# Optimization experiments

Measured on AMD Instinct MI355X. Metric: run time of the kernel, lower is better.

The kernel has to match this reference:

```python
import jax, jax.numpy as jnp
import numpy as np

EPS = 1e-5

def gru_step(x, h, Wih, Whh, bih, bhh):
    # PyTorch GRU cell math. x:[B,C], h:[B,H], Wih:[3H,C], Whh:[3H,H]
    gi = x @ Wih.T + bih
    gh = h @ Whh.T + bhh
    ir, iz, inn = jnp.split(gi, 3, axis=-1)
    hr, hz, hn = jnp.split(gh, 3, axis=-1)
    r = jax.nn.sigmoid(ir + hr)
    z = jax.nn.sigmoid(iz + hz)
    n = jnp.tanh(inn + r * hn)
    return (1.0 - z) * n + z * h

def batchnorm_train(x, g, b):
    # x:[B,C]; training-mode BN over batch dim, biased variance
    mu = jnp.mean(x, axis=0)
    var = jnp.mean((x - mu) ** 2, axis=0)
    return g * (x - mu) / jnp.sqrt(var + EPS) + b

def setup_inputs() -> dict:
    B, Le, T = 256, 1024, 48
    Fe, Fd, G, R, H = 16, 16, 32, 16, 256
    Ce, Cd = Fe + R, Fd + R + 1  # 32, 33
    key = jax.random.key(0)
    ks = jax.random.split(key, 24)
    s = 0.05
    inp = {
        "X_Encoder": jax.random.normal(ks[0], (B, Le, Fe), jnp.float32),
        "X_Decoder": jax.random.normal(ks[1], (B, T, Fd), jnp.float32),
        "Xg_Encoder": jax.random.normal(ks[2], (B, Le, G), jnp.float32),
        "Xg_Decoder": jax.random.normal(ks[3], (B, T, G), jnp.float32),
        # global feature reducers
        "Wg_enc": jax.random.normal(ks[4], (R, G), jnp.float32) * s,
        "bg_enc": jnp.zeros((R,), jnp.float32),
        "Wg_dec": jax.random.normal(ks[5], (R, G), jnp.float32) * s,
        "bg_dec": jnp.zeros((R,), jnp.float32),
        # encoder GRU + output head
        "enc_Wih": jax.random.normal(ks[6], (3 * H, Ce), jnp.float32) * s,
        "enc_Whh": jax.random.normal(ks[7], (3 * H, H), jnp.float32) * s,
        "enc_bih": jnp.zeros((3 * H,), jnp.float32),
        "enc_bhh": jnp.zeros((3 * H,), jnp.float32),
        "enc_Wo": jax.random.normal(ks[8], (1, H), jnp.float32) * s,
        "enc_bo": jnp.zeros((1,), jnp.float32),
        # decoder GRU + output head
        "dec_Wih": jax.random.normal(ks[9], (3 * H, Cd), jnp.float32) * s,
        "dec_Whh": jax.random.normal(ks[10], (3 * H, H), jnp.float32) * s,
        "dec_bih": jnp.zeros((3 * H,), jnp.float32),
        "dec_bhh": jnp.zeros((3 * H,), jnp.float32),
        "dec_Wo": jax.random.normal(ks[11], (1, H), jnp.float32) * s,
        "dec_bo": jnp.zeros((1,), jnp.float32),
        # BatchNorm params: BN_1 and per-step BN_layers (T of them)
        "bn1_g": jnp.ones((Cd,), jnp.float32),
        "bn1_b": jnp.zeros((Cd,), jnp.float32),
        "bnT_g": jnp.ones((T, Cd), jnp.float32),
        "bnT_b": jnp.zeros((T, Cd), jnp.float32),
    }
    return inp

def reference(X_Encoder, X_Decoder, Xg_Encoder, Xg_Decoder,
              Wg_enc, bg_enc, Wg_dec, bg_dec,
              enc_Wih, enc_Whh, enc_bih, enc_bhh, enc_Wo, enc_bo,
              dec_Wih, dec_Whh, dec_bih, dec_bhh, dec_Wo, dec_bo,
              bn1_g, bn1_b, bnT_g, bnT_b):
    B, Le, _ = X_Encoder.shape
    T = X_Decoder.shape[1]
    H = enc_Whh.shape[1]
    # batched global-feature reduction (replaces nested per-element loops)
    enc_in = jnp.concatenate([X_Encoder, Xg_Encoder @ Wg_enc.T + bg_enc], axis=2)  # [B,Le,Ce]
    dec_wg = jnp.concatenate([X_Decoder, Xg_Decoder @ Wg_dec.T + bg_dec], axis=2)  # [B,T,Fd+R]
    # encoder: sequential GRU over Le steps
    def estep(h, x):
        return gru_step(x, h, enc_Wih, enc_Whh, enc_bih, enc_bhh), None
    h0 = jnp.zeros((B, H), enc_in.dtype)
    h_enc, _ = jax.lax.scan(estep, h0, jnp.swapaxes(enc_in, 0, 1))
    enc_out = h_enc @ enc_Wo.T + enc_bo  # [B,1]
    # first decoder input: concat + BN_1 (train mode); dropout p=0 -> identity
    dec_in0 = batchnorm_train(jnp.concatenate([dec_wg[:, 0], enc_out], axis=1), bn1_g, bn1_b)
    # next-step exogenous inputs, padded with zeros for the (unused) last step
    next_x = jnp.concatenate([dec_wg[:, 1:], jnp.zeros((B, 1, dec_wg.shape[2]), dec_wg.dtype)], axis=1)
    next_x = jnp.swapaxes(next_x, 0, 1)  # [T,B,Fd+R]
    def dstep(carry, xs):
        h, dinp = carry
        nx, g, b = xs
        h = gru_step(dinp, h, dec_Wih, dec_Whh, dec_bih, dec_bhh)
        out = h @ dec_Wo.T + dec_bo  # [B,1]
        new_in = batchnorm_train(jnp.concatenate([nx, out], axis=1), g, b)
        return (h, new_in), out
    (_, _), outs = jax.lax.scan(dstep, (h_enc, dec_in0), (next_x, bnT_g, bnT_b))
    return jnp.swapaxes(outs, 0, 1)  # [B,T,1]
```

## Files before the change

kernel.cpp:

```cpp
#include <hip/hip_runtime.h>
#include <math.h>

typedef _Float16 f16;
typedef _Float16 f16x8 __attribute__((ext_vector_type(8)));
typedef float f32x4 __attribute__((ext_vector_type(4)));

#define MFMA16(A_, B_, C_) __builtin_amdgcn_mfma_f32_16x16x32_f16((A_), (B_), (C_), 0, 0, 0)
#define SWZ(m) ((((m) & 7) ^ (((m) & 8) >> 2)) << 4)

__device__ __forceinline__ float rcpf_(float x) { return __builtin_amdgcn_rcpf(x); }
__device__ __forceinline__ float rsqf_(float x) { return __builtin_amdgcn_rsqf(x); }
__device__ __forceinline__ float sigf(float x) { return rcpf_(1.0f + __expf(-x)); }
__device__ __forceinline__ float tanhf_(float x) { return 1.0f - 2.0f * rcpf_(__expf(2.0f * x) + 1.0f); }

static const size_t OFF_ENCIN = 0;
static const size_t OFF_DECIN = 16777216;
static const size_t OFF_WENC  = OFF_DECIN + 786432;
static const size_t OFF_WDEC  = OFF_WENC + 442368;
static const size_t OFF_W32   = OFF_WDEC + 442368;
static const size_t OFF_BE    = OFF_W32 + 3072;
static const size_t OFF_BD    = OFF_BE + 4096;
static const size_t OFF_HENC  = OFF_BD + 4096;
static const size_t OFF_EOUT  = OFF_HENC + 131072;
static const size_t OFF_XST   = OFF_EOUT + 1024;
static const size_t OFF_OST   = OFF_XST + 12288;
static const size_t OFF_CNT   = OFF_OST + 512;

struct P {
  const float *Xe, *Xd, *Xge, *Xgd, *Wge, *bge, *Wgd, *bgd;
  const float *eWih, *eWhh, *ebih, *ebhh, *eWo, *ebo;
  const float *dWih, *dWhh, *dbih, *dbhh, *dWo, *dbo;
  const float *bn1g, *bn1b, *bnTg, *bnTb;
  f16 *encin, *decin, *wencf, *wdecf;
  float *w32, *bE, *bD;
  f16 *henc;
  float *eout, *xst, *ost;
  int *cnt;
  float *out;
};

__global__ void prep1(P p) {
  const int blk = blockIdx.x, tid = threadIdx.x;
  __shared__ float swg[512];
  __shared__ float sbg[16];
  if (blk < 1024) {
    for (int i = tid; i < 512; i += 256) swg[i] = p.Wge[i];
    if (tid < 16) sbg[tid] = p.bge[tid];
    __syncthreads();
    const int i = blk * 256 + tid;
    const int b = i >> 10, t = i & 1023;
    const float* xg = p.Xge + (size_t)(b * 1024 + t) * 32;
    const float* xe = p.Xe + (size_t)(b * 1024 + t) * 16;
    f16* o = p.encin + (size_t)(t * 256 + b) * 32;
    float xgv[32];
#pragma unroll
    for (int k = 0; k < 32; ++k) xgv[k] = xg[k];
#pragma unroll
    for (int c = 0; c < 16; ++c) o[c] = (f16)xe[c];
#pragma unroll 4
    for (int r = 0; r < 16; ++r) {
      float acc = sbg[r];
#pragma unroll
      for (int k = 0; k < 32; ++k) acc += swg[r * 32 + k] * xgv[k];
      o[16 + r] = (f16)acc;
    }
  } else if (blk < 1072) {
    for (int i = tid; i < 512; i += 256) swg[i] = p.Wgd[i];
    if (tid < 16) sbg[tid] = p.bgd[tid];
    __syncthreads();
    const int i = (blk - 1024) * 256 + tid;
// ... 29 lines not shown
    const int kt = i / 3072, r2 = i - kt * 3072;
    const int nt = r2 >> 6, l = r2 & 63;
    const int n = nt * 16 + (l & 15), g = l >> 4;
    f16* o = p.wdecf + (size_t)i * 8;
#pragma unroll
    for (int j = 0; j < 8; ++j) {
      const int k = g * 8 + j;
      o[j] = (f16)((kt == 0) ? p.dWih[n * 33 + k] : p.dWhh[n * 256 + (kt - 1) * 32 + k]);
    }
  } else if (blk == 1288) {
    for (int i = tid; i < 768; i += 256) p.w32[i] = p.dWih[i * 33 + 32];
    for (int i = tid; i < 128; i += 256) p.ost[i] = 0.f;
    if (tid < 64) p.cnt[tid] = 0;
  } else if (blk == 1289) {
    for (int i = tid; i < 1024; i += 256) {
      float v;
      if (i < 512) v = p.ebih[i] + p.ebhh[i];
      else if (i < 768) v = p.ebih[i];
      else v = p.ebhh[i - 256];
      p.bE[i] = v;
    }
  } else {
    for (int i = tid; i < 1024; i += 256) {
      float v;
      if (i < 512) v = p.dbih[i] + p.dbhh[i];
      else if (i < 768) v = p.dbih[i];
      else v = p.dbhh[i - 256];
      p.bD[i] = v;
    }
  }
}

__global__ void prep2(P p) {
  const int i = blockIdx.x * 256 + threadIdx.x;
  if (i >= 48 * 32) return;
  const int s = i >> 5, c = i & 31;
  float s1 = 0.f, s2 = 0.f;
  for (int b = 0; b < 256; ++b) {
    const float v = (float)p.decin[(size_t)(s * 256 + b) * 32 + c];
    s1 += v; s2 += v * v;
  }
  const float mu = s1 * (1.0f / 256.0f);
  p.xst[i * 2] = mu;
  p.xst[i * 2 + 1] = s2 * (1.0f / 256.0f) - mu * mu;
}

__global__ __launch_bounds__(512, 2) void enc_kernel(P p) {
  __shared__ f16 sWL[49152];
  __shared__ f16 sH[8192];
  __shared__ float sRed[512];
  const int tid = threadIdx.x;
  const int l = tid & 63, w = tid >> 6;
  const int g = l >> 4, m16 = l & 15;
  const int swzA = SWZ(m16);
  const int bg = blockIdx.x * 16;

  {
    const int4* src = (const int4*)(p.wencf + 172032);
    int4* dst = (int4*)sWL;
#pragma unroll
    for (int i = 0; i < 12; ++i) dst[tid + i * 512] = src[tid + i * 512];
  }
  {
    int* hz = (int*)sH;
#pragma unroll
    for (int i = 0; i < 8; ++i) hz[tid + i * 512] = 0;
  }
  const int nts[6] = {w, 8 + w, 16 + w, 24 + w, 32 + w, 40 + w};
  f16x8 Wr[7][6];
#pragma unroll
  for (int kt = 0; kt < 7; ++kt)
#pragma unroll
    for (int i = 0; i < 6; ++i)
      Wr[kt][i] = *(const f16x8*)(p.wencf + ((size_t)(kt * 48 + nts[i]) * 64 + l) * 8);
  const int J1 = 16 * w + m16, J2 = 128 + J1;
  const float br1 = p.bE[J1], bz1 = p.bE[256 + J1], bi1 = p.bE[512 + J1], bh1 = p.bE[768 + J1];
  const float br2 = p.bE[J2], bz2 = p.bE[256 + J2], bi2 = p.bE[512 + J2], bh2 = p.bE[768 + J2];
  float hp1[4] = {0.f, 0.f, 0.f, 0.f}, hp2[4] = {0.f, 0.f, 0.f, 0.f};
  __syncthreads();

  int ph = 0;
  f16x8 xf = *(const f16x8*)(p.encin + (size_t)(bg + m16) * 32 + 8 * g);
#pragma unroll 1
  for (int t = 0; t < 1024; ++t) {
    const int tn = (t < 1023) ? t + 1 : t;
    const f16x8 xn = *(const f16x8*)(p.encin + (size_t)(tn * 256 + bg + m16) * 32 + 8 * g);
    f32x4 aR0 = {br1, br1, br1, br1}, aR1 = {br2, br2, br2, br2};
    f32x4 aZ0 = {bz1, bz1, bz1, bz1}, aZ1 = {bz2, bz2, bz2, bz2};
    f32x4 aNi0 = {bi1, bi1, bi1, bi1}, aNi1 = {bi2, bi2, bi2, bi2};
    f32x4 aNh0 = {bh1, bh1, bh1, bh1}, aNh1 = {bh2, bh2, bh2, bh2};
    aR0 = MFMA16(xf, Wr[0][0], aR0);
    aR1 = MFMA16(xf, Wr[0][1], aR1);
    aZ0 = MFMA16(xf, Wr[0][2], aZ0);
    aZ1 = MFMA16(xf, Wr[0][3], aZ1);
    aNi0 = MFMA16(xf, Wr[0][4], aNi0);
    aNi1 = MFMA16(xf, Wr[0][5], aNi1);
#pragma unroll
    for (int kk = 1; kk <= 6; ++kk) {
      const f16x8 a = *(const f16x8*)((const char*)sH + ph * 8192 + m16 * 512 +
                                      ((64 * (kk - 1) + 16 * g) ^ swzA));
      aR0 = MFMA16(a, Wr[kk][0], aR0);
      aR1 = MFMA16(a, Wr[kk][1], aR1);
      aZ0 = MFMA16(a, Wr[kk][2], aZ0);
      aZ1 = MFMA16(a, Wr[kk][3], aZ1);
      aNh0 = MFMA16(a, Wr[kk][4], aNh0);
      aNh1 = MFMA16(a, Wr[kk][5], aNh1);
    }
#pragma unroll
    for (int kk = 7; kk <= 8; ++kk) {
      const f16x8 a = *(const f16x8*)((const char*)sH + ph * 8192 + m16 * 512 +
                                      ((64 * (kk - 1) + 16 * g) ^ swzA));
      const char* wb = (const char*)sWL + (kk - 7) * 49152;
      const f16x8 q0 = *(const f16x8*)(wb + (nts[0] * 64 + l) * 16);
      const f16x8 q1 = *(const f16x8*)(wb + (nts[1] * 64 + l) * 16);
      const f16x8 q2 = *(const f16x8*)(wb + (nts[2] * 64 + l) * 16);
      const f16x8 q3 = *(const f16x8*)(wb + (nts[3] * 64 + l) * 16);
      const f16x8 q4 = *(const f16x8*)(wb + (nts[4] * 64 + l) * 16);
      const f16x8 q5 = *(const f16x8*)(wb + (nts[5] * 64 + l) * 16);
      aR0 = MFMA16(a, q0, aR0);
      aR1 = MFMA16(a, q1, aR1);
      aZ0 = MFMA16(a, q2, aZ0);
      aZ1 = MFMA16(a, q3, aZ1);
      aNh0 = MFMA16(a, q4, aNh0);
      aNh1 = MFMA16(a, q5, aNh1);
    }
    {
      char* hw = (char*)sH + (ph ^ 1) * 8192;
#pragma unroll
      for (int q = 0; q < 4; ++q) {
        const int m = 4 * g + q;
        const int sw = SWZ(m);
        const float r1 = sigf(aR0[q]);
        const float z1 = sigf(aZ0[q]);
        const float n1 = tanhf_(aNi0[q] + r1 * aNh0[q]);
        const f16 h1 = (f16)(n1 + z1 * (hp1[q] - n1));
        hp1[q] = (float)h1;
        *(f16*)(hw + m * 512 + ((2 * J1) ^ sw)) = h1;
        const float r2 = sigf(aR1[q]);
        const float z2 = sigf(aZ1[q]);
        const float n2 = tanhf_(aNi1[q] + r2 * aNh1[q]);
        const f16 h2 = (f16)(n2 + z2 * (hp2[q] - n2));
        hp2[q] = (float)h2;
        *(f16*)(hw + m * 512 + ((2 * J2) ^ sw)) = h2;
      }
    }
    __syncthreads();
    ph ^= 1;
    xf = xn;
  }
  {
    const char* hb = (const char*)sH + ph * 8192;
    const int m = tid & 15, grp = tid >> 4;
    const f16x8 hv = *(const f16x8*)(hb + m * 512 + ((16 * grp) ^ SWZ(m)));
    *(f16x8*)(p.henc + (size_t)(bg + m) * 256 + 8 * grp) = hv;
    float part = 0.f;
#pragma unroll
    for (int jj = 0; jj < 8; ++jj) part += (float)hv[jj] * p.eWo[8 * grp + jj];
    sRed[m * 32 + grp] = part;
    __syncthreads();
    if (tid < 16) {
      float o = p.ebo[0];
#pragma unroll 8
      for (int k = 0; k < 32; ++k) o += sRed[tid * 32 + k];
      p.eout[bg + tid] = o;
    }
  }
}

__global__ __launch_bounds__(512, 2) void dec_kernel(P p) {
  __shared__ f16 sWL[49152];
  __shared__ f16 sH[8192];
  __shared__ f16 sDin[1024];
  __shared__ float sRed[512];
  __shared__ float sOutv[16];
  __shared__ float sO32[16];
  const int tid = threadIdx.x;
  const int l = tid & 63, w = tid >> 6;
  const int g = l >> 4, m16 = l & 15;
  const int sw16 = (m16 & 7) << 4;
  const int swzA = SWZ(m16);
  const int bg = blockIdx.x * 16;

  {
    const int4* src = (const int4*)(p.wdecf + 172032);
    int4* dst = (int4*)sWL;
#pragma unroll
    for (int i = 0; i < 12; ++i) dst[tid + i * 512] = src[tid + i * 512];
  }
  {
    const int m = tid & 15, grp = tid >> 4;
    const f16x8 hv = *(const f16x8*)(p.henc + (size_t)(bg + m) * 256 + 8 * grp);
    *(f16x8*)((char*)sH + m * 512 + ((16 * grp) ^ SWZ(m))) = hv;
  }
  if (tid < 128) ((int4*)sDin)[tid] = int4{0, 0, 0, 0};
  const int nts[6] = {w, 8 + w, 16 + w, 24 + w, 32 + w, 40 + w};
  f16x8 Wr[7][6];
#pragma unroll
  for (int kt = 0; kt < 7; ++kt)
#pragma unroll
    for (int i = 0; i < 6; ++i)
      Wr[kt][i] = *(const f16x8*)(p.wdecf + ((size_t)(kt * 48 + nts[i]) * 64 + l) * 8);
  const int J1 = 16 * w + m16, J2 = 128 + J1;
  const float br1 = p.bD[J1], bz1 = p.bD[256 + J1], bi1 = p.bD[512 + J1], bh1 = p.bD[768 + J1];
  const float br2 = p.bD[J2], bz2 = p.bD[256 + J2], bi2 = p.bD[512 + J2], bh2 = p.bD[768 + J2];
  const float w32r1 = p.w32[J1], w32z1 = p.w32[256 + J1], w32n1 = p.w32[512 + J1];
  const float w32r2 = p.w32[J2], w32z2 = p.w32[256 + J2], w32n2 = p.w32[512 + J2];
  float hp1[4], hp2[4];
#pragma unroll
  for (int q = 0; q < 4; ++q) {
    hp1[q] = (float)p.henc[(size_t)(bg + 4 * g + q) * 256 + J1];
    hp2[q] = (float)p.henc[(size_t)(bg + 4 * g + q) * 256 + J2];
  }
  if (tid < 16) sOutv[tid] = p.eout[bg + tid];
  __syncthreads();
  if (tid == 0) {
    float s1 = 0.f, s2 = 0.f;
#pragma unroll
    for (int k = 0; k < 16; ++k) { const float v = sOutv[k]; s1 += v; s2 += v * v; }
    atomicAdd(&p.ost[0], s1);
    atomicAdd(&p.ost[1], s2);
    __hip_atomic_fetch_add(&p.cnt[0], 1, __ATOMIC_RELEASE, __HIP_MEMORY_SCOPE_AGENT);
  }

  int ph = 0;
#pragma unroll 1
  for (int t = 0; t < 48; ++t) {
    const int mp = tid & 15, cp = tid >> 4;
    const float xq = (float)p.decin[((size_t)t * 256 + bg + mp) * 32 + cp];
    const float mx = p.xst[(t * 32 + cp) * 2], vx = p.xst[(t * 32 + cp) * 2 + 1];
    const float gc = (t == 0) ? p.bn1g[cp] : p.bnTg[(t - 1) * 33 + cp];
    const float bc = (t == 0) ? p.bn1b[cp] : p.bnTb[(t - 1) * 33 + cp];
    float gK = 0.f, bK = 0.f;
    if (tid < 16) {
      gK = (t == 0) ? p.bn1g[32] : p.bnTg[(t - 1) * 33 + 32];
      bK = (t == 0) ? p.bn1b[32] : p.bnTb[(t - 1) * 33 + 32];
    }
    f32x4 aR0 = {br1, br1, br1, br1}, aR1 = {br2, br2, br2, br2};
    f32x4 aZ0 = {bz1, bz1, bz1, bz1}, aZ1 = {bz2, bz2, bz2, bz2};
    f32x4 aNi0 = {bi1, bi1, bi1, bi1}, aNi1 = {bi2, bi2, bi2, bi2};
    f32x4 aNh0 = {bh1, bh1, bh1, bh1}, aNh1 = {bh2, bh2, bh2, bh2};
#pragma unroll
    for (int kk = 1; kk <= 6; ++kk) {
      const f16x8 a = *(const f16x8*)((const char*)sH + ph * 8192 + m16 * 512 +
                                      ((64 * (kk - 1) + 16 * g) ^ swzA));
      aR0 = MFMA16(a, Wr[kk][0], aR0);
      aR1 = MFMA16(a, Wr[kk][1], aR1);
      aZ0 = MFMA16(a, Wr[kk][2], aZ0);
      aZ1 = MFMA16(a, Wr[kk][3], aZ1);
      aNh0 = MFMA16(a, Wr[kk][4], aNh0);
      aNh1 = MFMA16(a, Wr[kk][5], aNh1);
    }
#pragma unroll
    for (int kk = 7; kk <= 8; ++kk) {
      const f16x8 a = *(const f16x8*)((const char*)sH + ph * 8192 + m16 * 512 +
                                      ((64 * (kk - 1) + 16 * g) ^ swzA));
      const char* wb = (const char*)sWL + (kk - 7) * 49152;
      const f16x8 q0 = *(const f16x8*)(wb + (nts[0] * 64 + l) * 16);
      const f16x8 q1 = *(const f16x8*)(wb + (nts[1] * 64 + l) * 16);
      const f16x8 q2 = *(const f16x8*)(wb + (nts[2] * 64 + l) * 16);
      const f16x8 q3 = *(const f16x8*)(wb + (nts[3] * 64 + l) * 16);
      const f16x8 q4 = *(const f16x8*)(wb + (nts[4] * 64 + l) * 16);
      const f16x8 q5 = *(const f16x8*)(wb + (nts[5] * 64 + l) * 16);
      aR0 = MFMA16(a, q0, aR0);
      aR1 = MFMA16(a, q1, aR1);
      aZ0 = MFMA16(a, q2, aZ0);
      aZ1 = MFMA16(a, q3, aZ1);
      aNh0 = MFMA16(a, q4, aNh0);
      aNh1 = MFMA16(a, q5, aNh1);
    }
    if (tid == 0) {
      while (__hip_atomic_load(&p.cnt[t], __ATOMIC_ACQUIRE, __HIP_MEMORY_SCOPE_AGENT) < 16)
        __builtin_amdgcn_s_sleep(1);
    }
    __syncthreads();
    if (tid < 16) {
      const float S1 = __hip_atomic_load(&p.ost[2 * t], __ATOMIC_RELAXED, __HIP_MEMORY_SCOPE_AGENT);
      const float S2 = __hip_atomic_load(&p.ost[2 * t + 1], __ATOMIC_RELAXED, __HIP_MEMORY_SCOPE_AGENT);
      const float mu = S1 * (1.0f / 256.0f);
      const float var = S2 * (1.0f / 256.0f) - mu * mu;
      sO32[tid] = gK * (sOutv[tid] - mu) * rsqf_(var + 1e-5f) + bK;
    }
    *(f16*)((char*)sDin + mp * 128 + ((2 * cp) ^ ((mp & 7) << 4))) =
        (f16)(gc * (xq - mx) * rsqf_(vx + 1e-5f) + bc);
    __syncthreads();
    {
      const f16x8 a = *(const f16x8*)((const char*)sDin + m16 * 128 + ((16 * g) ^ sw16));
      aR0 = MFMA16(a, Wr[0][0], aR0);
      aR1 = MFMA16(a, Wr[0][1], aR1);
      aZ0 = MFMA16(a, Wr[0][2], aZ0);
      aZ1 = MFMA16(a, Wr[0][3], aZ1);
      aNi0 = MFMA16(a, Wr[0][4], aNi0);
      aNi1 = MFMA16(a, Wr[0][5], aNi1);
    }
    {
      char* hw = (char*)sH + (ph ^ 1) * 8192;
#pragma unroll
      for (int q = 0; q < 4; ++q) {
        const int m = 4 * g + q;
        const int sw = SWZ(m);
        const float o32m = sO32[m];
        const float r1 = sigf(aR0[q] + o32m * w32r1);
        const float z1 = sigf(aZ0[q] + o32m * w32z1);
        const float n1 = tanhf_(aNi0[q] + o32m * w32n1 + r1 * aNh0[q]);
        const f16 h1 = (f16)(n1 + z1 * (hp1[q] - n1));
        hp1[q] = (float)h1;
        *(f16*)(hw + m * 512 + ((2 * J1) ^ sw)) = h1;
        const float r2 = sigf(aR1[q] + o32m * w32r2);
        const float z2 = sigf(aZ1[q] + o32m * w32z2);
        const float n2 = tanhf_(aNi1[q] + o32m * w32n2 + r2 * aNh1[q]);
        const f16 h2 = (f16)(n2 + z2 * (hp2[q] - n2));
        hp2[q] = (float)h2;
        *(f16*)(hw + m * 512 + ((2 * J2) ^ sw)) = h2;
      }
    }
    __syncthreads();
    {
      const int m = tid & 15, grp = tid >> 4;
      const char* hb = (const char*)sH + (ph ^ 1) * 8192;
      const f16x8 hv = *(const f16x8*)(hb + m * 512 + ((16 * grp) ^ SWZ(m)));
      float part = 0.f;
#pragma unroll
      for (int jj = 0; jj < 8; ++jj) part += (float)hv[jj] * p.dWo[8 * grp + jj];
      sRed[m * 32 + grp] = part;
    }
    __syncthreads();
    if (tid < 16) {
      float o = p.dbo[0];
#pragma unroll 8
      for (int k = 0; k < 32; ++k) o += sRed[tid * 32 + k];
      p.out[(size_t)(bg + tid) * 48 + t] = o;
      sOutv[tid] = o;
    }
    __syncthreads();
    if (t < 47 && tid == 0) {
      float s1 = 0.f, s2 = 0.f;
#pragma unroll
      for (int k = 0; k < 16; ++k) { const float v = sOutv[k]; s1 += v; s2 += v * v; }
      atomicAdd(&p.ost[2 * (t + 1)], s1);
      atomicAdd(&p.ost[2 * (t + 1) + 1], s2);
      __hip_atomic_fetch_add(&p.cnt[t + 1], 1, __ATOMIC_RELEASE, __HIP_MEMORY_SCOPE_AGENT);
    }
    ph ^= 1;
  }
}

extern "C" void kernel_launch(void* const* d_in, const int* in_sizes, int n_in,
                              void* d_out, int out_size, void* d_ws, size_t ws_size,
                              hipStream_t stream) {
  char* ws = (char*)d_ws;
// ... 4 lines not shown
  p.Xgd  = (const float*)d_in[3];
  p.Wge  = (const float*)d_in[4];
  p.bge  = (const float*)d_in[5];
  p.Wgd  = (const float*)d_in[6];
  p.bgd  = (const float*)d_in[7];
  p.eWih = (const float*)d_in[8];
  p.eWhh = (const float*)d_in[9];
  p.ebih = (const float*)d_in[10];
  p.ebhh = (const float*)d_in[11];
  p.eWo  = (const float*)d_in[12];
  p.ebo  = (const float*)d_in[13];
  p.dWih = (const float*)d_in[14];
  p.dWhh = (const float*)d_in[15];
  p.dbih = (const float*)d_in[16];
  p.dbhh = (const float*)d_in[17];
  p.dWo  = (const float*)d_in[18];
  p.dbo  = (const float*)d_in[19];
  p.bn1g = (const float*)d_in[20];
  p.bn1b = (const float*)d_in[21];
  p.bnTg = (const float*)d_in[22];
  p.bnTb = (const float*)d_in[23];
  p.encin = (f16*)(ws + OFF_ENCIN);
  p.decin = (f16*)(ws + OFF_DECIN);
  p.wencf = (f16*)(ws + OFF_WENC);
  p.wdecf = (f16*)(ws + OFF_WDEC);
  p.w32   = (float*)(ws + OFF_W32);
  p.bE    = (float*)(ws + OFF_BE);
  p.bD    = (float*)(ws + OFF_BD);
  p.henc  = (f16*)(ws + OFF_HENC);
  p.eout  = (float*)(ws + OFF_EOUT);
  p.xst   = (float*)(ws + OFF_XST);
  p.ost   = (float*)(ws + OFF_OST);
  p.cnt   = (int*)(ws + OFF_CNT);
  p.out   = (float*)d_out;

  prep1<<<dim3(1291), dim3(256), 0, stream>>>(p);
  prep2<<<dim3(6), dim3(256), 0, stream>>>(p);
  enc_kernel<<<dim3(16), dim3(512), 0, stream>>>(p);
  dec_kernel<<<dim3(16), dim3(512), 0, stream>>>(p);
}
```

Measured before the change: 3.677 ms.

## Stream spilled GRU weight tiles from global memory instead of LDS

Drops the LDS copy of the last two K-tiles of the recurrent weights in the encoder and decoder. prep2 now writes those tiles into a per-wave contiguous global layout, duplicated twice so that ph*49152 offsets index a valid copy. The loop loads them into registers at the top of each step, which frees LDS and lets the load latency overlap the earlier MFMAs. Biases move out of the accumulator initialisation into the gate math, and the input MFMA moves after the recurrent MFMAs. The cost is a global or L2 load per step on the serial critical path and higher register pressure.

Result: faster. 3.381 ms (-8.0%).

```diff
diff --git a/kernel.cpp b/kernel.cpp
--- a/kernel.cpp
+++ b/kernel.cpp
@@ -25,6 +25,8 @@
 static const size_t OFF_XST   = OFF_EOUT + 1024;
 static const size_t OFF_OST   = OFF_XST + 12288;
 static const size_t OFF_CNT   = OFF_OST + 512;
+static const size_t OFF_WSE   = OFF_CNT + 256;
+static const size_t OFF_WSD   = OFF_WSE + 196608;
 
 struct P {
   const float *Xe, *Xd, *Xge, *Xgd, *Wge, *bge, *Wgd, *bgd;
@@ -36,6 +38,7 @@
   f16 *henc;
   float *eout, *xst, *ost;
   int *cnt;
+  f16 *wse, *wsd;
   float *out;
 };
 
@@ -131,21 +134,38 @@
 }
 
 __global__ void prep2(P p) {
-  const int i = blockIdx.x * 256 + threadIdx.x;
-  if (i >= 48 * 32) return;
-  const int s = i >> 5, c = i & 31;
-  float s1 = 0.f, s2 = 0.f;
-  for (int b = 0; b < 256; ++b) {
-    const float v = (float)p.decin[(size_t)(s * 256 + b) * 32 + c];
-    s1 += v; s2 += v * v;
-  }
-  const float mu = s1 * (1.0f / 256.0f);
-  p.xst[i * 2] = mu;
-  p.xst[i * 2 + 1] = s2 * (1.0f / 256.0f) - mu * mu;
+  const int blk = blockIdx.x, tid = threadIdx.x;
+  if (blk < 6) {
+    const int i = blk * 256 + tid;
+    if (i >= 48 * 32) return;
+    const int s = i >> 5, c = i & 31;
+    float s1 = 0.f, s2 = 0.f;
+    for (int b = 0; b < 256; ++b) {
+      const float v = (float)p.decin[(size_t)(s * 256 + b) * 32 + c];
+      s1 += v; s2 += v * v;
+    }
+    const float mu = s1 * (1.0f / 256.0f);
+    p.xst[i * 2] = mu;
+    p.xst[i * 2 + 1] = s2 * (1.0f / 256.0f) - mu * mu;
+  } else {
+    const int idx = (blk - 6) * 256 + tid;
+    const int sel = idx >= 6144;
+    const int fi = sel ? idx - 6144 : idx;
+    const int wv = fi / 768;
+    const int r = fi - wv * 768;
+    const int i8 = r >> 6, l = r & 63;
+    const int kt = (i8 >= 6) ? 8 : 7;
+    const int j = (i8 >= 6) ? i8 - 6 : i8;
+    const int nt = j * 8 + wv;
+    const f16* src = (sel ? p.wdecf : p.wencf) + ((size_t)((kt * 48 + nt) * 64 + l)) * 8;
+    f16* dst = (sel ? p.wsd : p.wse) + (size_t)fi * 8;
+    const f16x8 v = *(const f16x8*)src;
+    *(f16x8*)dst = v;
+    *(f16x8*)(dst + 49152) = v;
+  }
 }
 
 __global__ __launch_bounds__(512, 2) void enc_kernel(P p) {
-  __shared__ f16 sWL[49152];
   __shared__ f16 sH[8192];
   __shared__ float sRed[512];
   const int tid = threadIdx.x;
@@ -155,12 +175,6 @@
   const int bg = blockIdx.x * 16;
 
   {
-    const int4* src = (const int4*)(p.wencf + 172032);
-    int4* dst = (int4*)sWL;
-#pragma unroll
-    for (int i = 0; i < 12; ++i) dst[tid + i * 512] = src[tid + i * 512];
-  }
-  {
     int* hz = (int*)sH;
 #pragma unroll
     for (int i = 0; i < 8; ++i) hz[tid + i * 512] = 0;
@@ -172,6 +186,9 @@
 #pragma unroll
     for (int i = 0; i < 6; ++i)
       Wr[kt][i] = *(const f16x8*)(p.wencf + ((size_t)(kt * 48 + nts[i]) * 64 + l) * 8);
+  const f16* sb0 = p.wse + ((size_t)(w * 12 + 0) * 64 + l) * 8;
+  const f16* sb1 = p.wse + ((size_t)(w * 12 + 4) * 64 + l) * 8;
+  const f16* sb2 = p.wse + ((size_t)(w * 12 + 8) * 64 + l) * 8;
   const int J1 = 16 * w + m16, J2 = 128 + J1;
   const float br1 = p.bE[J1], bz1 = p.bE[256 + J1], bi1 = p.bE[512 + J1], bh1 = p.bE[768 + J1];
   const float br2 = p.bE[J2], bz2 = p.bE[256 + J2], bi2 = p.bE[512 + J2], bh2 = p.bE[768 + J2];
@@ -179,21 +196,19 @@
   __syncthreads();
 
   int ph = 0;
-  f16x8 xf = *(const f16x8*)(p.encin + (size_t)(bg + m16) * 32 + 8 * g);
 #pragma unroll 1
   for (int t = 0; t < 1024; ++t) {
-    const int tn = (t < 1023) ? t + 1 : t;
-    const f16x8 xn = *(const f16x8*)(p.encin + (size_t)(tn * 256 + bg + m16) * 32 + 8 * g);
-    f32x4 aR0 = {br1, br1, br1, br1}, aR1 = {br2, br2, br2, br2};
-    f32x4 aZ0 = {bz1, bz1, bz1, bz1}, aZ1 = {bz2, bz2, bz2, bz2};
-    f32x4 aNi0 = {bi1, bi1, bi1, bi1}, aNi1 = {bi2, bi2, bi2, bi2};
-    f32x4 aNh0 = {bh1, bh1, bh1, bh1}, aNh1 = {bh2, bh2, bh2, bh2};
-    aR0 = MFMA16(xf, Wr[0][0], aR0);
-    aR1 = MFMA16(xf, Wr[0][1], aR1);
-    aZ0 = MFMA16(xf, Wr[0][2], aZ0);
-    aZ1 = MFMA16(xf, Wr[0][3], aZ1);
-    aNi0 = MFMA16(xf, Wr[0][4], aNi0);
-    aNi1 = MFMA16(xf, Wr[0][5], aNi1);
+    const int so = ph * 49152;
+    f16x8 qW[12];
+#pragma unroll
+    for (int k = 0; k < 4; ++k) qW[k] = *(const f16x8*)(sb0 + so + k * 512);
+#pragma unroll
+    for (int k = 0; k < 4; ++k) qW[4 + k] = *(const f16x8*)(sb1 + so + k * 512);
+#pragma unroll
+    for (int k = 0; k < 4; ++k) qW[8 + k] = *(const f16x8*)(sb2 + so + k * 512);
+    const f16x8 xf = *(const f16x8*)(p.encin + ((size_t)t * 256 + bg + m16) * 32 + 8 * g);
+    f32x4 aR0 = {0,0,0,0}, aR1 = {0,0,0,0}, aZ0 = {0,0,0,0}, aZ1 = {0,0,0,0};
+    f32x4 aNh0 = {0,0,0,0}, aNh1 = {0,0,0,0};
 #pragma unroll
     for (int kk = 1; kk <= 6; ++kk) {
       const f16x8 a = *(const f16x8*)((const char*)sH + ph * 8192 + m16 * 512 +
@@ -209,35 +224,36 @@
     for (int kk = 7; kk <= 8; ++kk) {
       const f16x8 a = *(const f16x8*)((const char*)sH + ph * 8192 + m16 * 512 +
                                       ((64 * (kk - 1) + 16 * g) ^ swzA));
-      const char* wb = (const char*)sWL + (kk - 7) * 49152;
-      const f16x8 q0 = *(const f16x8*)(wb + (nts[0] * 64 + l) * 16);
-      const f16x8 q1 = *(const f16x8*)(wb + (nts[1] * 64 + l) * 16);
-      const f16x8 q2 = *(const f16x8*)(wb + (nts[2] * 64 + l) * 16);
-      const f16x8 q3 = *(const f16x8*)(wb + (nts[3] * 64 + l) * 16);
-      const f16x8 q4 = *(const f16x8*)(wb + (nts[4] * 64 + l) * 16);
-      const f16x8 q5 = *(const f16x8*)(wb + (nts[5] * 64 + l) * 16);
-      aR0 = MFMA16(a, q0, aR0);
-      aR1 = MFMA16(a, q1, aR1);
-      aZ0 = MFMA16(a, q2, aZ0);
-      aZ1 = MFMA16(a, q3, aZ1);
-      aNh0 = MFMA16(a, q4, aNh0);
-      aNh1 = MFMA16(a, q5, aNh1);
-    }
+      const int qb = (kk - 7) * 6;
+      aR0 = MFMA16(a, qW[qb + 0], aR0);
+      aR1 = MFMA16(a, qW[qb + 1], aR1);
+      aZ0 = MFMA16(a, qW[qb + 2], aZ0);
+      aZ1 = MFMA16(a, qW[qb + 3], aZ1);
+      aNh0 = MFMA16(a, qW[qb + 4], aNh0);
+      aNh1 = MFMA16(a, qW[qb + 5], aNh1);
+    }
+    f32x4 aNi0 = {0,0,0,0}, aNi1 = {0,0,0,0};
+    aR0 = MFMA16(xf, Wr[0][0], aR0);
+    aR1 = MFMA16(xf, Wr[0][1], aR1);
+    aZ0 = MFMA16(xf, Wr[0][2], aZ0);
+    aZ1 = MFMA16(xf, Wr[0][3], aZ1);
+    aNi0 = MFMA16(xf, Wr[0][4], aNi0);
+    aNi1 = MFMA16(xf, Wr[0][5], aNi1);
     {
       char* hw = (char*)sH + (ph ^ 1) * 8192;
 #pragma unroll
       for (int q = 0; q < 4; ++q) {
         const int m = 4 * g + q;
         const int sw = SWZ(m);
-        const float r1 = sigf(aR0[q]);
-        const float z1 = sigf(aZ0[q]);
-        const float n1 = tanhf_(aNi0[q] + r1 * aNh0[q]);
+        const float r1 = sigf(aR0[q] + br1);
+        const float z1 = sigf(aZ0[q] + bz1);
+        const float n1 = tanhf_(aNi0[q] + bi1 + r1 * (aNh0[q] + bh1));
         const f16 h1 = (f16)(n1 + z1 * (hp1[q] - n1));
         hp1[q] = (float)h1;
         *(f16*)(hw + m * 512 + ((2 * J1) ^ sw)) = h1;
-        const float r2 = sigf(aR1[q]);
-        const float z2 = sigf(aZ1[q]);
-        const float n2 = tanhf_(aNi1[q] + r2 * aNh1[q]);
+        const float r2 = sigf(aR1[q] + br2);
+        const float z2 = sigf(aZ1[q] + bz2);
+        const float n2 = tanhf_(aNi1[q] + bi2 + r2 * (aNh1[q] + bh2));
         const f16 h2 = (f16)(n2 + z2 * (hp2[q] - n2));
         hp2[q] = (float)h2;
         *(f16*)(hw + m * 512 + ((2 * J2) ^ sw)) = h2;
@@ -245,7 +261,6 @@
     }
     __syncthreads();
     ph ^= 1;
-    xf = xn;
   }
   {
     const char* hb = (const char*)sH + ph * 8192;
@@ -267,7 +282,6 @@
 }
 
 __global__ __launch_bounds__(512, 2) void dec_kernel(P p) {
-  __shared__ f16 sWL[49152];
   __shared__ f16 sH[8192];
   __shared__ f16 sDin[1024];
   __shared__ float sRed[512];
@@ -281,12 +295,6 @@
   const int bg = blockIdx.x * 16;
 
   {
-    const int4* src = (const int4*)(p.wdecf + 172032);
-    int4* dst = (int4*)sWL;
-#pragma unroll
-    for (int i = 0; i < 12; ++i) dst[tid + i * 512] = src[tid + i * 512];
-  }
-  {
     const int m = tid & 15, grp = tid >> 4;
     const f16x8 hv = *(const f16x8*)(p.henc + (size_t)(bg + m) * 256 + 8 * grp);
     *(f16x8*)((char*)sH + m * 512 + ((16 * grp) ^ SWZ(m))) = hv;
@@ -299,6 +307,9 @@
 #pragma unroll
     for (int i = 0; i < 6; ++i)
       Wr[kt][i] = *(const f16x8*)(p.wdecf + ((size_t)(kt * 48 + nts[i]) * 64 + l) * 8);
+  const f16* sb0 = p.wsd + ((size_t)(w * 12 + 0) * 64 + l) * 8;
+  const f16* sb1 = p.wsd + ((size_t)(w * 12 + 4) * 64 + l) * 8;
+  const f16* sb2 = p.wsd + ((size_t)(w * 12 + 8) * 64 + l) * 8;
   const int J1 = 16 * w + m16, J2 = 128 + J1;
   const float br1 = p.bD[J1], bz1 = p.bD[256 + J1], bi1 = p.bD[512 + J1], bh1 = p.bD[768 + J1];
   const float br2 = p.bD[J2], bz2 = p.bD[256 + J2], bi2 = p.bD[512 + J2], bh2 = p.bD[768 + J2];
@@ -324,6 +335,14 @@
   int ph = 0;
 #pragma unroll 1
   for (int t = 0; t < 48; ++t) {
+    const int so = ph * 49152;
+    f16x8 qW[12];
+#pragma unroll
+    for (int k = 0; k < 4; ++k) qW[k] = *(const f16x8*)(sb0 + so + k * 512);
+#pragma unroll
+    for (int k = 0; k < 4; ++k) qW[4 + k] = *(const f16x8*)(sb1 + so + k * 512);
+#pragma unroll
+    for (int k = 0; k < 4; ++k) qW[8 + k] = *(const f16x8*)(sb2 + so + k * 512);
     const int mp = tid & 15, cp = tid >> 4;
     const float xq = (float)p.decin[((size_t)t * 256 + bg + mp) * 32 + cp];
     const float mx = p.xst[(t * 32 + cp) * 2], vx = p.xst[(t * 32 + cp) * 2 + 1];
@@ -334,10 +353,8 @@
       gK = (t == 0) ? p.bn1g[32] : p.bnTg[(t - 1) * 33 + 32];
       bK = (t == 0) ? p.bn1b[32] : p.bnTb[(t - 1) * 33 + 32];
     }
-    f32x4 aR0 = {br1, br1, br1, br1}, aR1 = {br2, br2, br2, br2};
-    f32x4 aZ0 = {bz1, bz1, bz1, bz1}, aZ1 = {bz2, bz2, bz2, bz2};
-    f32x4 aNi0 = {bi1, bi1, bi1, bi1}, aNi1 = {bi2, bi2, bi2, bi2};
-    f32x4 aNh0 = {bh1, bh1, bh1, bh1}, aNh1 = {bh2, bh2, bh2, bh2};
+    f32x4 aR0 = {0,0,0,0}, aR1 = {0,0,0,0}, aZ0 = {0,0,0,0}, aZ1 = {0,0,0,0};
+    f32x4 aNh0 = {0,0,0,0}, aNh1 = {0,0,0,0};
 #pragma unroll
     for (int kk = 1; kk <= 6; ++kk) {
       const f16x8 a = *(const f16x8*)((const char*)sH + ph * 8192 + m16 * 512 +
@@ -353,19 +370,13 @@
     for (int kk = 7; kk <= 8; ++kk) {
       const f16x8 a = *(const f16x8*)((const char*)sH + ph * 8192 + m16 * 512 +
                                       ((64 * (kk - 1) + 16 * g) ^ swzA));
-      const char* wb = (const char*)sWL + (kk - 7) * 49152;
-      const f16x8 q0 = *(const f16x8*)(wb + (nts[0] * 64 + l) * 16);
-      const f16x8 q1 = *(const f16x8*)(wb + (nts[1] * 64 + l) * 16);
-      const f16x8 q2 = *(const f16x8*)(wb + (nts[2] * 64 + l) * 16);
-      const f16x8 q3 = *(const f16x8*)(wb + (nts[3] * 64 + l) * 16);
-      const f16x8 q4 = *(const f16x8*)(wb + (nts[4] * 64 + l) * 16);
-      const f16x8 q5 = *(const f16x8*)(wb + (nts[5] * 64 + l) * 16);
-      aR0 = MFMA16(a, q0, aR0);
-      aR1 = MFMA16(a, q1, aR1);
-      aZ0 = MFMA16(a, q2, aZ0);
-      aZ1 = MFMA16(a, q3, aZ1);
-      aNh0 = MFMA16(a, q4, aNh0);
-      aNh1 = MFMA16(a, q5, aNh1);
+      const int qb = (kk - 7) * 6;
+      aR0 = MFMA16(a, qW[qb + 0], aR0);
+      aR1 = MFMA16(a, qW[qb + 1], aR1);
+      aZ0 = MFMA16(a, qW[qb + 2], aZ0);
+      aZ1 = MFMA16(a, qW[qb + 3], aZ1);
+      aNh0 = MFMA16(a, qW[qb + 4], aNh0);
+      aNh1 = MFMA16(a, qW[qb + 5], aNh1);
     }
     if (tid == 0) {
       while (__hip_atomic_load(&p.cnt[t], __ATOMIC_ACQUIRE, __HIP_MEMORY_SCOPE_AGENT) < 16)
@@ -382,6 +393,7 @@
     *(f16*)((char*)sDin + mp * 128 + ((2 * cp) ^ ((mp & 7) << 4))) =
         (f16)(gc * (xq - mx) * rsqf_(vx + 1e-5f) + bc);
     __syncthreads();
+    f32x4 aNi0 = {0,0,0,0}, aNi1 = {0,0,0,0};
     {
       const f16x8 a = *(const f16x8*)((const char*)sDin + m16 * 128 + ((16 * g) ^ sw16));
       aR0 = MFMA16(a, Wr[0][0], aR0);
@@ -398,15 +410,15 @@
         const int m = 4 * g + q;
         const int sw = SWZ(m);
         const float o32m = sO32[m];
-        const float r1 = sigf(aR0[q] + o32m * w32r1);
-        const float z1 = sigf(aZ0[q] + o32m * w32z1);
-        const float n1 = tanhf_(aNi0[q] + o32m * w32n1 + r1 * aNh0[q]);
+        const float r1 = sigf(aR0[q] + br1 + o32m * w32r1);
+        const float z1 = sigf(aZ0[q] + bz1 + o32m * w32z1);
+        const float n1 = tanhf_(aNi0[q] + bi1 + o32m * w32n1 + r1 * (aNh0[q] + bh1));
         const f16 h1 = (f16)(n1 + z1 * (hp1[q] - n1));
         hp1[q] = (float)h1;
         *(f16*)(hw + m * 512 + ((2 * J1) ^ sw)) = h1;
-        const float r2 = sigf(aR1[q] + o32m * w32r2);
-        const float z2 = sigf(aZ1[q] + o32m * w32z2);
-        const float n2 = tanhf_(aNi1[q] + o32m * w32n2 + r2 * aNh1[q]);
+        const float r2 = sigf(aR1[q] + br2 + o32m * w32r2);
+        const float z2 = sigf(aZ1[q] + bz2 + o32m * w32z2);
+        const float n2 = tanhf_(aNi1[q] + bi2 + o32m * w32n2 + r2 * (aNh1[q] + bh2));
         const f16 h2 = (f16)(n2 + z2 * (hp2[q] - n2));
         hp2[q] = (float)h2;
         *(f16*)(hw + m * 512 + ((2 * J2) ^ sw)) = h2;
@@ -484,10 +496,12 @@
   p.xst   = (float*)(ws + OFF_XST);
   p.ost   = (float*)(ws + OFF_OST);
   p.cnt   = (int*)(ws + OFF_CNT);
+  p.wse   = (f16*)(ws + OFF_WSE);
+  p.wsd   = (f16*)(ws + OFF_WSD);
   p.out   = (float*)d_out;
 
   prep1<<<dim3(1291), dim3(256), 0, stream>>>(p);
-  prep2<<<dim3(6), dim3(256), 0, stream>>>(p);
+  prep2<<<dim3(54), dim3(256), 0, stream>>>(p);
   enc_kernel<<<dim3(16), dim3(512), 0, stream>>>(p);
   dec_kernel<<<dim3(16), dim3(512), 0, stream>>>(p);
 }
```

## Split GRU recurrence across 16 waves per block, halving per-wave gate tiles

Applied to the files above, without the earlier changes.

Encoder and decoder kernels now launch 1024 threads per block instead of 512. Each wave owns one 16-column hidden tile (3 gate accumulators) rather than two, which halves the serial MFMA chain and register-resident weights per wave. The input-projection MFMAs are also moved after the recurrent ones in the encoder, and the next-step input prefetch is dropped. In exchange the per-step barrier spans more waves and the reduction and BN phases need tid<512 guards, leaving half the threads idle there.

Measured after the change: 3.559 ms. -3.2%, faster.

```diff
diff --git a/kernel.cpp b/kernel.cpp
--- a/kernel.cpp
+++ b/kernel.cpp
@@ -144,7 +144,7 @@
   p.xst[i * 2 + 1] = s2 * (1.0f / 256.0f) - mu * mu;
 }
 
-__global__ __launch_bounds__(512, 2) void enc_kernel(P p) {
+__global__ __launch_bounds__(1024, 4) void enc_kernel(P p) {
   __shared__ f16 sWL[49152];
   __shared__ f16 sH[8192];
   __shared__ float sRed[512];
@@ -158,104 +158,81 @@
     const int4* src = (const int4*)(p.wencf + 172032);
     int4* dst = (int4*)sWL;
 #pragma unroll
-    for (int i = 0; i < 12; ++i) dst[tid + i * 512] = src[tid + i * 512];
+    for (int i = 0; i < 6; ++i) dst[tid + i * 1024] = src[tid + i * 1024];
   }
   {
     int* hz = (int*)sH;
 #pragma unroll
-    for (int i = 0; i < 8; ++i) hz[tid + i * 512] = 0;
-  }
-  const int nts[6] = {w, 8 + w, 16 + w, 24 + w, 32 + w, 40 + w};
-  f16x8 Wr[7][6];
-#pragma unroll
-  for (int kt = 0; kt < 7; ++kt)
-#pragma unroll
-    for (int i = 0; i < 6; ++i)
-      Wr[kt][i] = *(const f16x8*)(p.wencf + ((size_t)(kt * 48 + nts[i]) * 64 + l) * 8);
-  const int J1 = 16 * w + m16, J2 = 128 + J1;
-  const float br1 = p.bE[J1], bz1 = p.bE[256 + J1], bi1 = p.bE[512 + J1], bh1 = p.bE[768 + J1];
-  const float br2 = p.bE[J2], bz2 = p.bE[256 + J2], bi2 = p.bE[512 + J2], bh2 = p.bE[768 + J2];
-  float hp1[4] = {0.f, 0.f, 0.f, 0.f}, hp2[4] = {0.f, 0.f, 0.f, 0.f};
+    for (int i = 0; i < 4; ++i) hz[tid + i * 1024] = 0;
+  }
+  f16x8 Wr[7][3];
+#pragma unroll
+  for (int kt = 0; kt < 7; ++kt) {
+    Wr[kt][0] = *(const f16x8*)(p.wencf + ((size_t)(kt * 48 + w) * 64 + l) * 8);
+    Wr[kt][1] = *(const f16x8*)(p.wencf + ((size_t)(kt * 48 + 16 + w) * 64 + l) * 8);
+    Wr[kt][2] = *(const f16x8*)(p.wencf + ((size_t)(kt * 48 + 32 + w) * 64 + l) * 8);
+  }
+  const int u = 16 * w + m16;
+  const float br = p.bE[u], bz = p.bE[256 + u], bi = p.bE[512 + u], bh = p.bE[768 + u];
+  float hp[4] = {0.f, 0.f, 0.f, 0.f};
   __syncthreads();
 
   int ph = 0;
-  f16x8 xf = *(const f16x8*)(p.encin + (size_t)(bg + m16) * 32 + 8 * g);
 #pragma unroll 1
   for (int t = 0; t < 1024; ++t) {
-    const int tn = (t < 1023) ? t + 1 : t;
-    const f16x8 xn = *(const f16x8*)(p.encin + (size_t)(tn * 256 + bg + m16) * 32 + 8 * g);
-    f32x4 aR0 = {br1, br1, br1, br1}, aR1 = {br2, br2, br2, br2};
-    f32x4 aZ0 = {bz1, bz1, bz1, bz1}, aZ1 = {bz2, bz2, bz2, bz2};
-    f32x4 aNi0 = {bi1, bi1, bi1, bi1}, aNi1 = {bi2, bi2, bi2, bi2};
-    f32x4 aNh0 = {bh1, bh1, bh1, bh1}, aNh1 = {bh2, bh2, bh2, bh2};
-    aR0 = MFMA16(xf, Wr[0][0], aR0);
-    aR1 = MFMA16(xf, Wr[0][1], aR1);
-    aZ0 = MFMA16(xf, Wr[0][2], aZ0);
-    aZ1 = MFMA16(xf, Wr[0][3], aZ1);
-    aNi0 = MFMA16(xf, Wr[0][4], aNi0);
-    aNi1 = MFMA16(xf, Wr[0][5], aNi1);
+    const f16x8 xf = *(const f16x8*)(p.encin + ((size_t)t * 256 + bg + m16) * 32 + 8 * g);
+    f32x4 aR = {br, br, br, br}, aZ = {bz, bz, bz, bz}, aNh = {bh, bh, bh, bh};
 #pragma unroll
     for (int kk = 1; kk <= 6; ++kk) {
       const f16x8 a = *(const f16x8*)((const char*)sH + ph * 8192 + m16 * 512 +
                                       ((64 * (kk - 1) + 16 * g) ^ swzA));
-      aR0 = MFMA16(a, Wr[kk][0], aR0);
-      aR1 = MFMA16(a, Wr[kk][1], aR1);
-      aZ0 = MFMA16(a, Wr[kk][2], aZ0);
-      aZ1 = MFMA16(a, Wr[kk][3], aZ1);
-      aNh0 = MFMA16(a, Wr[kk][4], aNh0);
-      aNh1 = MFMA16(a, Wr[kk][5], aNh1);
+      aR = MFMA16(a, Wr[kk][0], aR);
+      aZ = MFMA16(a, Wr[kk][1], aZ);
+      aNh = MFMA16(a, Wr[kk][2], aNh);
     }
 #pragma unroll
     for (int kk = 7; kk <= 8; ++kk) {
       const f16x8 a = *(const f16x8*)((const char*)sH + ph * 8192 + m16 * 512 +
                                       ((64 * (kk - 1) + 16 * g) ^ swzA));
       const char* wb = (const char*)sWL + (kk - 7) * 49152;
-      const f16x8 q0 = *(const f16x8*)(wb + (nts[0] * 64 + l) * 16);
-      const f16x8 q1 = *(const f16x8*)(wb + (nts[1] * 64 + l) * 16);
-      const f16x8 q2 = *(const f16x8*)(wb + (nts[2] * 64 + l) * 16);
-      const f16x8 q3 = *(const f16x8*)(wb + (nts[3] * 64 + l) * 16);
-      const f16x8 q4 = *(const f16x8*)(wb + (nts[4] * 64 + l) * 16);
-      const f16x8 q5 = *(const f16x8*)(wb + (nts[5] * 64 + l) * 16);
-      aR0 = MFMA16(a, q0, aR0);
-      aR1 = MFMA16(a, q1, aR1);
-      aZ0 = MFMA16(a, q2, aZ0);
-      aZ1 = MFMA16(a, q3, aZ1);
-      aNh0 = MFMA16(a, q4, aNh0);
-      aNh1 = MFMA16(a, q5, aNh1);
-    }
+      const f16x8 q0 = *(const f16x8*)(wb + ((0 + w) * 64 + l) * 16);
+      const f16x8 q1 = *(const f16x8*)(wb + ((16 + w) * 64 + l) * 16);
+      const f16x8 q2 = *(const f16x8*)(wb + ((32 + w) * 64 + l) * 16);
+      aR = MFMA16(a, q0, aR);
+      aZ = MFMA16(a, q1, aZ);
+      aNh = MFMA16(a, q2, aNh);
+    }
+    f32x4 aNi = {bi, bi, bi, bi};
+    aR = MFMA16(xf, Wr[0][0], aR);
+    aZ = MFMA16(xf, Wr[0][1], aZ);
+    aNi = MFMA16(xf, Wr[0][2], aNi);
     {
       char* hw = (char*)sH + (ph ^ 1) * 8192;
 #pragma unroll
       for (int q = 0; q < 4; ++q) {
         const int m = 4 * g + q;
-        const int sw = SWZ(m);
-        const float r1 = sigf(aR0[q]);
-        const float z1 = sigf(aZ0[q]);
-        const float n1 = tanhf_(aNi0[q] + r1 * aNh0[q]);
-        const f16 h1 = (f16)(n1 + z1 * (hp1[q] - n1));
-        hp1[q] = (float)h1;
-        *(f16*)(hw + m * 512 + ((2 * J1) ^ sw)) = h1;
-        const float r2 = sigf(aR1[q]);
-        const float z2 = sigf(aZ1[q]);
-        const float n2 = tanhf_(aNi1[q] + r2 * aNh1[q]);
-        const f16 h2 = (f16)(n2 + z2 * (hp2[q] - n2));
-        hp2[q] = (float)h2;
-        *(f16*)(hw + m * 512 + ((2 * J2) ^ sw)) = h2;
+        const float r = sigf(aR[q]);
+        const float z = sigf(aZ[q]);
+        const float n = tanhf_(aNi[q] + r * aNh[q]);
+        const f16 h = (f16)(n + z * (hp[q] - n));
+        hp[q] = (float)h;
+        *(f16*)(hw + m * 512 + ((2 * u) ^ SWZ(m))) = h;
       }
     }
     __syncthreads();
     ph ^= 1;
-    xf = xn;
   }
   {
     const char* hb = (const char*)sH + ph * 8192;
-    const int m = tid & 15, grp = tid >> 4;
-    const f16x8 hv = *(const f16x8*)(hb + m * 512 + ((16 * grp) ^ SWZ(m)));
-    *(f16x8*)(p.henc + (size_t)(bg + m) * 256 + 8 * grp) = hv;
-    float part = 0.f;
-#pragma unroll
-    for (int jj = 0; jj < 8; ++jj) part += (float)hv[jj] * p.eWo[8 * grp + jj];
-    sRed[m * 32 + grp] = part;
+    if (tid < 512) {
+      const int m = tid & 15, grp = tid >> 4;
+      const f16x8 hv = *(const f16x8*)(hb + m * 512 + ((16 * grp) ^ SWZ(m)));
+      *(f16x8*)(p.henc + (size_t)(bg + m) * 256 + 8 * grp) = hv;
+      float part = 0.f;
+#pragma unroll
+      for (int jj = 0; jj < 8; ++jj) part += (float)hv[jj] * p.eWo[8 * grp + jj];
+      sRed[m * 32 + grp] = part;
+    }
     __syncthreads();
     if (tid < 16) {
       float o = p.ebo[0];
@@ -266,7 +243,7 @@
   }
 }
 
-__global__ __launch_bounds__(512, 2) void dec_kernel(P p) {
+__global__ __launch_bounds__(1024, 4) void dec_kernel(P p) {
   __shared__ f16 sWL[49152];
   __shared__ f16 sH[8192];
   __shared__ f16 sDin[1024];
@@ -284,32 +261,28 @@
     const int4* src = (const int4*)(p.wdecf + 172032);
     int4* dst = (int4*)sWL;
 #pragma unroll
-    for (int i = 0; i < 12; ++i) dst[tid + i * 512] = src[tid + i * 512];
-  }
-  {
+    for (int i = 0; i < 6; ++i) dst[tid + i * 1024] = src[tid + i * 1024];
+  }
+  if (tid < 512) {
     const int m = tid & 15, grp = tid >> 4;
     const f16x8 hv = *(const f16x8*)(p.henc + (size_t)(bg + m) * 256 + 8 * grp);
     *(f16x8*)((char*)sH + m * 512 + ((16 * grp) ^ SWZ(m))) = hv;
   }
   if (tid < 128) ((int4*)sDin)[tid] = int4{0, 0, 0, 0};
-  const int nts[6] = {w, 8 + w, 16 + w, 24 + w, 32 + w, 40 + w};
-  f16x8 Wr[7][6];
-#pragma unroll
-  for (int kt = 0; kt < 7; ++kt)
-#pragma unroll
-    for (int i = 0; i < 6; ++i)
-      Wr[kt][i] = *(const f16x8*)(p.wdecf + ((size_t)(kt * 48 + nts[i]) * 64 + l) * 8);
-  const int J1 = 16 * w + m16, J2 = 128 + J1;
-  const float br1 = p.bD[J1], bz1 = p.bD[256 + J1], bi1 = p.bD[512 + J1], bh1 = p.bD[768 + J1];
-  const float br2 = p.bD[J2], bz2 = p.bD[256 + J2], bi2 = p.bD[512 + J2], bh2 = p.bD[768 + J2];
-  const float w32r1 = p.w32[J1], w32z1 = p.w32[256 + J1], w32n1 = p.w32[512 + J1];
-  const float w32r2 = p.w32[J2], w32z2 = p.w32[256 + J2], w32n2 = p.w32[512 + J2];
-  float hp1[4], hp2[4];
-#pragma unroll
-  for (int q = 0; q < 4; ++q) {
-    hp1[q] = (float)p.henc[(size_t)(bg + 4 * g + q) * 256 + J1];
-    hp2[q] = (float)p.henc[(size_t)(bg + 4 * g + q) * 256 + J2];
-  }
+  f16x8 Wr[7][3];
+#pragma unroll
+  for (int kt = 0; kt < 7; ++kt) {
+    Wr[kt][0] = *(const f16x8*)(p.wdecf + ((size_t)(kt * 48 + w) * 64 + l) * 8);
+    Wr[kt][1] = *(const f16x8*)(p.wdecf + ((size_t)(kt * 48 + 16 + w) * 64 + l) * 8);
+    Wr[kt][2] = *(const f16x8*)(p.wdecf + ((size_t)(kt * 48 + 32 + w) * 64 + l) * 8);
+  }
+  const int u = 16 * w + m16;
+  const float br = p.bD[u], bz = p.bD[256 + u], bi = p.bD[512 + u], bh = p.bD[768 + u];
+  const float w32r = p.w32[u], w32z = p.w32[256 + u], w32n = p.w32[512 + u];
+  float hp[4];
+#pragma unroll
+  for (int q = 0; q < 4; ++q)
+    hp[q] = (float)p.henc[(size_t)(bg + 4 * g + q) * 256 + u];
   if (tid < 16) sOutv[tid] = p.eout[bg + tid];
   __syncthreads();
   if (tid == 0) {
@@ -324,48 +297,40 @@
   int ph = 0;
 #pragma unroll 1
   for (int t = 0; t < 48; ++t) {
-    const int mp = tid & 15, cp = tid >> 4;
-    const float xq = (float)p.decin[((size_t)t * 256 + bg + mp) * 32 + cp];
-    const float mx = p.xst[(t * 32 + cp) * 2], vx = p.xst[(t * 32 + cp) * 2 + 1];
-    const float gc = (t == 0) ? p.bn1g[cp] : p.bnTg[(t - 1) * 33 + cp];
-    const float bc = (t == 0) ? p.bn1b[cp] : p.bnTb[(t - 1) * 33 + cp];
+    const int mp = tid & 15, cp = (tid >> 4) & 31;
+    float xq = 0.f, mx = 0.f, vx = 1.f, gc = 0.f, bc = 0.f;
+    if (tid < 512) {
+      xq = (float)p.decin[((size_t)t * 256 + bg + mp) * 32 + cp];
+      mx = p.xst[(t * 32 + cp) * 2];
+      vx = p.xst[(t * 32 + cp) * 2 + 1];
+      gc = (t == 0) ? p.bn1g[cp] : p.bnTg[(t - 1) * 33 + cp];
+      bc = (t == 0) ? p.bn1b[cp] : p.bnTb[(t - 1) * 33 + cp];
+    }
     float gK = 0.f, bK = 0.f;
     if (tid < 16) {
       gK = (t == 0) ? p.bn1g[32] : p.bnTg[(t - 1) * 33 + 32];
       bK = (t == 0) ? p.bn1b[32] : p.bnTb[(t - 1) * 33 + 32];
     }
-    f32x4 aR0 = {br1, br1, br1, br1}, aR1 = {br2, br2, br2, br2};
-    f32x4 aZ0 = {bz1, bz1, bz1, bz1}, aZ1 = {bz2, bz2, bz2, bz2};
-    f32x4 aNi0 = {bi1, bi1, bi1, bi1}, aNi1 = {bi2, bi2, bi2, bi2};
-    f32x4 aNh0 = {bh1, bh1, bh1, bh1}, aNh1 = {bh2, bh2, bh2, bh2};
+    f32x4 aR = {br, br, br, br}, aZ = {bz, bz, bz, bz}, aNh = {bh, bh, bh, bh};
 #pragma unroll
     for (int kk = 1; kk <= 6; ++kk) {
       const f16x8 a = *(const f16x8*)((const char*)sH + ph * 8192 + m16 * 512 +
                                       ((64 * (kk - 1) + 16 * g) ^ swzA));
-      aR0 = MFMA16(a, Wr[kk][0], aR0);
-      aR1 = MFMA16(a, Wr[kk][1], aR1);
-      aZ0 = MFMA16(a, Wr[kk][2], aZ0);
-      aZ1 = MFMA16(a, Wr[kk][3], aZ1);
-      aNh0 = MFMA16(a, Wr[kk][4], aNh0);
-      aNh1 = MFMA16(a, Wr[kk][5], aNh1);
+      aR = MFMA16(a, Wr[kk][0], aR);
+      aZ = MFMA16(a, Wr[kk][1], aZ);
+      aNh = MFMA16(a, Wr[kk][2], aNh);
     }
 #pragma unroll
     for (int kk = 7; kk <= 8; ++kk) {
       const f16x8 a = *(const f16x8*)((const char*)sH + ph * 8192 + m16 * 512 +
                                       ((64 * (kk - 1) + 16 * g) ^ swzA));
       const char* wb = (const char*)sWL + (kk - 7) * 49152;
-      const f16x8 q0 = *(const f16x8*)(wb + (nts[0] * 64 + l) * 16);
-      const f16x8 q1 = *(const f16x8*)(wb + (nts[1] * 64 + l) * 16);
-      const f16x8 q2 = *(const f16x8*)(wb + (nts[2] * 64 + l) * 16);
-      const f16x8 q3 = *(const f16x8*)(wb + (nts[3] * 64 + l) * 16);
-      const f16x8 q4 = *(const f16x8*)(wb + (nts[4] * 64 + l) * 16);
-      const f16x8 q5 = *(const f16x8*)(wb + (nts[5] * 64 + l) * 16);
-      aR0 = MFMA16(a, q0, aR0);
-      aR1 = MFMA16(a, q1, aR1);
-      aZ0 = MFMA16(a, q2, aZ0);
-      aZ1 = MFMA16(a, q3, aZ1);
-      aNh0 = MFMA16(a, q4, aNh0);
-      aNh1 = MFMA16(a, q5, aNh1);
+      const f16x8 q0 = *(const f16x8*)(wb + ((0 + w) * 64 + l) * 16);
+      const f16x8 q1 = *(const f16x8*)(wb + ((16 + w) * 64 + l) * 16);
+      const f16x8 q2 = *(const f16x8*)(wb + ((32 + w) * 64 + l) * 16);
+      aR = MFMA16(a, q0, aR);
+      aZ = MFMA16(a, q1, aZ);
+      aNh = MFMA16(a, q2, aNh);
     }
     if (tid == 0) {
       while (__hip_atomic_load(&p.cnt[t], __ATOMIC_ACQUIRE, __HIP_MEMORY_SCOPE_AGENT) < 16)
@@ -379,41 +344,33 @@
       const float var = S2 * (1.0f / 256.0f) - mu * mu;
       sO32[tid] = gK * (sOutv[tid] - mu) * rsqf_(var + 1e-5f) + bK;
     }
-    *(f16*)((char*)sDin + mp * 128 + ((2 * cp) ^ ((mp & 7) << 4))) =
-        (f16)(gc * (xq - mx) * rsqf_(vx + 1e-5f) + bc);
-    __syncthreads();
+    if (tid < 512)
+      *(f16*)((char*)sDin + mp * 128 + ((2 * cp) ^ ((mp & 7) << 4))) =
+          (f16)(gc * (xq - mx) * rsqf_(vx + 1e-5f) + bc);
+    __syncthreads();
+    f32x4 aNi = {bi, bi, bi, bi};
     {
       const f16x8 a = *(const f16x8*)((const char*)sDin + m16 * 128 + ((16 * g) ^ sw16));
-      aR0 = MFMA16(a, Wr[0][0], aR0);
-      aR1 = MFMA16(a, Wr[0][1], aR1);
-      aZ0 = MFMA16(a, Wr[0][2], aZ0);
-      aZ1 = MFMA16(a, Wr[0][3], aZ1);
-      aNi0 = MFMA16(a, Wr[0][4], aNi0);
-      aNi1 = MFMA16(a, Wr[0][5], aNi1);
+      aR = MFMA16(a, Wr[0][0], aR);
+      aZ = MFMA16(a, Wr[0][1], aZ);
+      aNi = MFMA16(a, Wr[0][2], aNi);
     }
     {
       char* hw = (char*)sH + (ph ^ 1) * 8192;
 #pragma unroll
       for (int q = 0; q < 4; ++q) {
         const int m = 4 * g + q;
-        const int sw = SWZ(m);
         const float o32m = sO32[m];
-        const float r1 = sigf(aR0[q] + o32m * w32r1);
-        const float z1 = sigf(aZ0[q] + o32m * w32z1);
-        const float n1 = tanhf_(aNi0[q] + o32m * w32n1 + r1 * aNh0[q]);
-        const f16 h1 = (f16)(n1 + z1 * (hp1[q] - n1));
-        hp1[q] = (float)h1;
-        *(f16*)(hw + m * 512 + ((2 * J1) ^ sw)) = h1;
-        const float r2 = sigf(aR1[q] + o32m * w32r2);
-        const float z2 = sigf(aZ1[q] + o32m * w32z2);
-        const float n2 = tanhf_(aNi1[q] + o32m * w32n2 + r2 * aNh1[q]);
-        const f16 h2 = (f16)(n2 + z2 * (hp2[q] - n2));
-        hp2[q] = (float)h2;
-        *(f16*)(hw + m * 512 + ((2 * J2) ^ sw)) = h2;
+        const float r = sigf(aR[q] + o32m * w32r);
+        const float z = sigf(aZ[q] + o32m * w32z);
+        const float n = tanhf_(aNi[q] + o32m * w32n + r * aNh[q]);
+        const f16 h = (f16)(n + z * (hp[q] - n));
+        hp[q] = (float)h;
+        *(f16*)(hw + m * 512 + ((2 * u) ^ SWZ(m))) = h;
       }
     }
     __syncthreads();
-    {
+    if (tid < 512) {
       const int m = tid & 15, grp = tid >> 4;
       const char* hb = (const char*)sH + (ph ^ 1) * 8192;
       const f16x8 hv = *(const f16x8*)(hb + m * 512 + ((16 * grp) ^ SWZ(m)));
@@ -488,6 +445,6 @@
 
   prep1<<<dim3(1291), dim3(256), 0, stream>>>(p);
   prep2<<<dim3(6), dim3(256), 0, stream>>>(p);
-  enc_kernel<<<dim3(16), dim3(512), 0, stream>>>(p);
-  dec_kernel<<<dim3(16), dim3(512), 0, stream>>>(p);
+  enc_kernel<<<dim3(16), dim3(1024), 0, stream>>>(p);
+  dec_kernel<<<dim3(16), dim3(1024), 0, stream>>>(p);
 }
```
